# Kernel optimization log

Hardware: AMD Instinct MI355X
Metric: run time of the kernel (lower is better)

The kernel has to match this reference:

```python
import jax, jax.numpy as jnp
import numpy as np

NUM_HEADS = 16
HEAD_DIM = 64  # hidden_size 1024 / 16 heads


def setup_inputs() -> dict:
    key = jax.random.key(0)
    k1, k2 = jax.random.split(key)
    B, S, D = 2, 2048, 1024
    hidden_states = jax.random.normal(k1, (B, S, D), dtype=jnp.float32)
    # fast_qkv: bias-free fused qkv projection + separate q/v biases (init zeros in torch)
    W_qkv = jax.random.normal(k2, (D, 3 * D), dtype=jnp.float32) * (1.0 / np.sqrt(D))
    q_bias = jnp.zeros((D,), dtype=jnp.float32)
    v_bias = jnp.zeros((D,), dtype=jnp.float32)
    return {"hidden_states": hidden_states, "W_qkv": W_qkv, "q_bias": q_bias, "v_bias": v_bias}


def reference(hidden_states, W_qkv, q_bias, v_bias):
    B, S, D = hidden_states.shape
    H, hd = NUM_HEADS, HEAD_DIM
    qkv = hidden_states @ W_qkv                      # (B,S,3D)
    q, k, v = jnp.split(qkv, 3, axis=-1)
    q = q + q_bias
    v = v + v_bias
    # (B,S,H,hd)
    q = q.reshape(B, S, H, hd)
    k = k.reshape(B, S, H, hd)
    v = v.reshape(B, S, H, hd)
    q = q / jnp.sqrt(jnp.asarray(hd, dtype=q.dtype))
    # full (B,H,S,S) score tensor, softmax in fp32 then cast back (matches torch)
    scores = jnp.einsum('bqhd,bkhd->bhqk', q, k)
    probs = jax.nn.softmax(scores.astype(jnp.float32), axis=-1).astype(v.dtype)
    ctx = jnp.einsum('bhqk,bkhd->bqhd', probs, v)    # (B,S,H,hd)
    return ctx.reshape(B, S, D)
```

## Files before the change

kernel.cpp:

```cpp
#include <hip/hip_runtime.h>
#include <hip/hip_bf16.h>

typedef _Float16 half_t;
typedef _Float16 h8 __attribute__((ext_vector_type(8)));
typedef _Float16 h4 __attribute__((ext_vector_type(4)));
typedef float f32x4 __attribute__((ext_vector_type(4)));
typedef float f4 __attribute__((ext_vector_type(4)));

#define DEVI __device__ __forceinline__

constexpr int NB = 2;
constexpr int S  = 2048;
constexpr int DM = 1024;
constexpr int NH = 16;
constexpr int HD = 64;
constexpr long M = (long)NB * S;
constexpr int N3 = 3 * DM;

DEVI f32x4 mfma16(h8 a, h8 b, f32x4 c) {
  return __builtin_amdgcn_mfma_f32_16x16x32_f16(a, b, c, 0, 0, 0);
}
DEVI f32x4 mfma16h(h4 a, h4 b, f32x4 c) {
  return __builtin_amdgcn_mfma_f32_16x16x16f16(a, b, c, 0, 0, 0);
}
DEVI h8 ld8h(const half_t* p) { return *(const h8*)p; }

#if __has_builtin(__builtin_amdgcn_exp2f)
DEVI float ex2(float x) { return __builtin_amdgcn_exp2f(x); }
#else
DEVI float ex2(float x) { float r; asm("v_exp_f32 %0, %1" : "=v"(r) : "v"(x)); return r; }
#endif

DEVI void gl_lds16(const half_t* g, half_t* l) {
  __builtin_amdgcn_global_load_lds(
      (const __attribute__((address_space(1))) void*)g,
      (__attribute__((address_space(3))) void*)l, 16, 0, 0);
}

__global__ void convert_h(const float* __restrict__ in, half_t* __restrict__ out) {
  const long i = ((long)blockIdx.x * 256 + threadIdx.x) * 8;
  const f4 a = *(const f4*)(in + i), b = *(const f4*)(in + i + 4);
  h8 r;
  #pragma unroll
  for (int k = 0; k < 4; k++) { r[k] = (half_t)a[k]; r[4 + k] = (half_t)b[k]; }
  *(h8*)(out + i) = r;
}

__global__ void transpose_w(const float* __restrict__ in, half_t* __restrict__ out) {
  __shared__ float tile[32][33];
  const int c0 = blockIdx.x * 32, r0 = blockIdx.y * 32;
  const int x = threadIdx.x, y = threadIdx.y;
  #pragma unroll
  for (int i = 0; i < 32; i += 8) tile[y + i][x] = in[(long)(r0 + y + i) * N3 + c0 + x];
  __syncthreads();
  #pragma unroll
  for (int i = 0; i < 32; i += 8)
    out[(long)(c0 + y + i) * DM + r0 + x] = (half_t)tile[x][y + i];
}

__global__ void transpose_v(const half_t* __restrict__ vb, half_t* __restrict__ vt) {
  __shared__ half_t tile[32][33];
  const int b = blockIdx.z >> 4, h = blockIdx.z & 15;
  const int d0 = blockIdx.x * 32, s0 = blockIdx.y * 32;
  const int x = threadIdx.x, y = threadIdx.y;
  const half_t* ip = vb + (long)b * S * DM + h * HD;
  half_t* op = vt + (long)(b * NH + h) * HD * S;
  #pragma unroll
  for (int i = 0; i < 32; i += 8) tile[y + i][x] = ip[(long)(s0 + y + i) * DM + d0 + x];
  __syncthreads();
  #pragma unroll
  for (int i = 0; i < 32; i += 8) op[(long)(d0 + y + i) * S + s0 + x] = tile[x][y + i];
}

__global__ __launch_bounds__(256) void qkv_gemm(
    const half_t* __restrict__ A, const half_t* __restrict__ Bt,
    const float* __restrict__ qbias, const float* __restrict__ vbias,
    half_t* __restrict__ Qf, half_t* __restrict__ Kf, half_t* __restrict__ Vb)
{
  constexpr int BM = 128, BN = 128, BK = 32;
  __shared__ alignas(16) half_t As[BM * BK];
  __shared__ alignas(16) half_t Bs[BN * BK];
  const int t = threadIdx.x, lane = t & 63, wave = t >> 6;
  const int quad = lane >> 4, l16 = lane & 15;
  const int id = blockIdx.x, xcd = id & 7, jj = id >> 3;
  const int m0 = (xcd * 4 + (jj & 3)) * BM;
  const int n0 = (jj >> 2) * BN;
  const int wm = (wave & 1) * 64, wn = (wave >> 1) * 64;

  const half_t* aP0 = A  + (long)(m0 + (t >> 2)) * DM + (t & 3) * 8;
  const half_t* aP1 = aP0 + (long)64 * DM;
  const half_t* bP0 = Bt + (long)(n0 + (t >> 2)) * DM + (t & 3) * 8;
  const half_t* bP1 = bP0 + (long)64 * DM;
  half_t* asW = As + wave * 512;
  half_t* bsW = Bs + wave * 512;

  f32x4 acc[4][4] = {};

  for (int k0 = 0; k0 < DM; k0 += BK) {
    __syncthreads();
    gl_lds16(aP0 + k0, asW);
    gl_lds16(aP1 + k0, asW + 2048);
    gl_lds16(bP0 + k0, bsW);
    gl_lds16(bP1 + k0, bsW + 2048);
    __builtin_amdgcn_s_waitcnt(0);
    __syncthreads();

    h8 af[4], bfr[4];
    #pragma unroll
    for (int i = 0; i < 4; i++) af[i]  = ld8h(&As[(wm + i * 16 + l16) * BK + quad * 8]);
    #pragma unroll
    for (int j = 0; j < 4; j++) bfr[j] = ld8h(&Bs[(wn + j * 16 + l16) * BK + quad * 8]);
    #pragma unroll
    for (int i = 0; i < 4; i++)
      #pragma unroll
      for (int j = 0; j < 4; j++)
        acc[i][j] = mfma16(af[i], bfr[j], acc[i][j]);
  }

  #pragma unroll
  for (int i = 0; i < 4; i++) {
    #pragma unroll
    for (int j = 0; j < 4; j++) {
      const int n = n0 + wn + j * 16 + l16;
      #pragma unroll
      for (int r = 0; r < 4; r++) {
        const long m = m0 + wm + i * 16 + quad * 4 + r;
        const float cv = acc[i][j][r];
        if (n < DM) {
          Qf[m * DM + n] = (half_t)((cv + qbias[n]) * 0.1803368801f);
        } else if (n < 2 * DM) {
          Kf[m * DM + (n - DM)] = (half_t)cv;
        } else {
          const int nv = n - 2 * DM;
          Vb[m * DM + nv] = (half_t)(cv + vbias[nv]);
        }
      }
    }
  }
}

__global__ __launch_bounds__(256) void attn(
    const half_t* __restrict__ Qf, const half_t* __restrict__ Kf,
    const half_t* __restrict__ Vt, float* __restrict__ out)
{
  constexpr int LK = 72, LV = 72;
  __shared__ alignas(16) half_t Ks[64 * LK];
  __shared__ alignas(16) half_t Vs[64 * LV];

  const int bh = blockIdx.y, b = bh >> 4, h = bh & 15;
  const int qt = blockIdx.x;
  const int t = threadIdx.x, lane = t & 63, wave = t >> 6;
  const int quad = lane >> 4, l16 = lane & 15;

  const long qrow0 = (long)b * S + qt * 128 + wave * 32;
  const half_t* qg = Qf + qrow0 * DM + h * HD;
  const half_t* kg = Kf + (long)b * S * DM + h * HD;
  const half_t* vg = Vt + (long)bh * HD * S;

  h8 bq[2][2];
  #pragma unroll
  for (int qi = 0; qi < 2; qi++)
    #pragma unroll
    for (int dh = 0; dh < 2; dh++)
      bq[qi][dh] = ld8h(&qg[(long)(qi * 16 + l16) * DM + dh * 32 + quad * 8]);

  const int r0s = t >> 3, c0s = (t & 7) * 8;
  const int r1s = 32 + r0s;
  h8 kreg[2], vreg[2];
  kreg[0] = ld8h(&kg[(long)r0s * DM + c0s]);
  kreg[1] = ld8h(&kg[(long)r1s * DM + c0s]);
  vreg[0] = ld8h(&vg[(long)r0s * S + c0s]);
  vreg[1] = ld8h(&vg[(long)r1s * S + c0s]);

  const f32x4 z4 = {0.f, 0.f, 0.f, 0.f};
  const h4 vones = {(half_t)1.f, (half_t)1.f, (half_t)1.f, (half_t)1.f};

  f32x4 O[2][4] = {};
  f32x4 lacc[2] = {};

  for (int kt = 0; kt < S / 64; ++kt) {
    __syncthreads();
    *(h8*)&Ks[r0s * LK + c0s] = kreg[0];
    *(h8*)&Ks[r1s * LK + c0s] = kreg[1];
    *(h8*)&Vs[r0s * LV + c0s] = vreg[0];
    *(h8*)&Vs[r1s * LV + c0s] = vreg[1];
    __syncthreads();

    if (kt < S / 64 - 1) {
      const long ko = (long)(kt + 1) * 64;
      kreg[0] = ld8h(&kg[(ko + r0s) * DM + c0s]);
      kreg[1] = ld8h(&kg[(ko + r1s) * DM + c0s]);
      vreg[0] = ld8h(&vg[(long)r0s * S + ko + c0s]);
      vreg[1] = ld8h(&vg[(long)r1s * S + ko + c0s]);
    }

    h4 pa[2][4];
    #pragma unroll
    for (int g = 0; g < 4; g++) {
      const h8 kf0 = ld8h(&Ks[(g * 16 + l16) * LK + quad * 8]);
      const h8 kf1 = ld8h(&Ks[(g * 16 + l16) * LK + 32 + quad * 8]);
      #pragma unroll
      for (int qi = 0; qi < 2; qi++) {
        f32x4 sc = mfma16(kf0, bq[qi][0], z4);
        sc = mfma16(kf1, bq[qi][1], sc);
        h4 pk;
        #pragma unroll
        for (int r = 0; r < 4; r++) pk[r] = (half_t)ex2(sc[r]);
        pa[qi][g] = pk;
      }
    }

    #pragma unroll
    for (int g = 0; g < 4; g++) {
      lacc[0] = mfma16h(pa[0][g], vones, lacc[0]);
      lacc[1] = mfma16h(pa[1][g], vones, lacc[1]);
    }

    #pragma unroll
    for (int j = 0; j < 4; j++) {
      #pragma unroll
      for (int g = 0; g < 4; g++) {
        const h4 vf = *(const h4*)&Vs[(j * 16 + l16) * LV + g * 16 + quad * 4];
        O[0][j] = mfma16h(pa[0][g], vf, O[0][j]);
        O[1][j] = mfma16h(pa[1][g], vf, O[1][j]);
      }
    }
  }

  #pragma unroll
  for (int qi = 0; qi < 2; qi++) {
    #pragma unroll
    for (int r = 0; r < 4; r++) {
      const float linv = 1.f / lacc[qi][r];
      const long srow = qrow0 + qi * 16 + quad * 4 + r;
      #pragma unroll
      for (int j = 0; j < 4; j++)
        out[srow * DM + h * HD + j * 16 + l16] = O[qi][j][r] * linv;
    }
  }
}

extern "C" void kernel_launch(void* const* d_in, const int* in_sizes, int n_in,
                              void* d_out, int out_size, void* d_ws, size_t ws_size,
                              hipStream_t stream) {
  (void)in_sizes; (void)n_in; (void)out_size; (void)ws_size;
  const float* hidden = (const float*)d_in[0];
  const float* W      = (const float*)d_in[1];
  const float* qbias  = (const float*)d_in[2];
  const float* vbias  = (const float*)d_in[3];
  float* out = (float*)d_out;

  half_t* ws = (half_t*)d_ws;
  half_t* Hb = ws;
  half_t* Wt = Hb + M * DM;
  half_t* Qf = Wt + (long)N3 * DM;
  half_t* Kf = Qf + M * DM;
  half_t* Vt = Kf + M * DM;

  half_t* Vb = (half_t*)d_out;

  convert_h<<<(int)(M * DM / (256 * 8)), 256, 0, stream>>>(hidden, Hb);
  transpose_w<<<dim3(N3 / 32, DM / 32), dim3(32, 8), 0, stream>>>(W, Wt);
  qkv_gemm<<<(N3 / 128) * (int)(M / 128), 256, 0, stream>>>(Hb, Wt, qbias, vbias, Qf, Kf, Vb);
  transpose_v<<<dim3(HD / 32, S / 32, NB * NH), dim3(32, 8), 0, stream>>>(Vb, Vt);
  attn<<<dim3(S / 128, NB * NH), 256, 0, stream>>>(Qf, Kf, Vt, out);
}
```

Measured before the change: 180.2 us.

## Load K/V fragments directly from global memory, drop LDS staging and barriers

The attention kernel no longer stages K and V tiles through shared memory with a register prefetch and two block barriers per iteration. Each wave now reads its MFMA operand fragments for K and V straight from global memory, relying on L1/L2 caching since all four waves read the same tile. This removes LDS traffic and synchronisation but multiplies global/cache load requests by the wave count. It also loses the explicit one-tile-ahead prefetch, so load latency may be exposed.

```diff
diff --git a/kernel.cpp b/kernel.cpp
--- a/kernel.cpp
+++ b/kernel.cpp
@@ -143,10 +143,6 @@
     const half_t* __restrict__ Qf, const half_t* __restrict__ Kf,
     const half_t* __restrict__ Vt, float* __restrict__ out)
 {
-  constexpr int LK = 72, LV = 72;
-  __shared__ alignas(16) half_t Ks[64 * LK];
-  __shared__ alignas(16) half_t Vs[64 * LV];
-
   const int bh = blockIdx.y, b = bh >> 4, h = bh & 15;
   const int qt = blockIdx.x;
   const int t = threadIdx.x, lane = t & 63, wave = t >> 6;
@@ -154,8 +150,8 @@
 
   const long qrow0 = (long)b * S + qt * 128 + wave * 32;
   const half_t* qg = Qf + qrow0 * DM + h * HD;
-  const half_t* kg = Kf + (long)b * S * DM + h * HD;
-  const half_t* vg = Vt + (long)bh * HD * S;
+  const half_t* kfb = Kf + ((long)b * S + l16) * DM + h * HD + quad * 8;
+  const half_t* vfb = Vt + (long)bh * HD * S + (long)l16 * S + quad * 4;
 
   h8 bq[2][2];
   #pragma unroll
@@ -164,14 +160,6 @@
     for (int dh = 0; dh < 2; dh++)
       bq[qi][dh] = ld8h(&qg[(long)(qi * 16 + l16) * DM + dh * 32 + quad * 8]);
 
-  const int r0s = t >> 3, c0s = (t & 7) * 8;
-  const int r1s = 32 + r0s;
-  h8 kreg[2], vreg[2];
-  kreg[0] = ld8h(&kg[(long)r0s * DM + c0s]);
-  kreg[1] = ld8h(&kg[(long)r1s * DM + c0s]);
-  vreg[0] = ld8h(&vg[(long)r0s * S + c0s]);
-  vreg[1] = ld8h(&vg[(long)r1s * S + c0s]);
-
   const f32x4 z4 = {0.f, 0.f, 0.f, 0.f};
   const h4 vones = {(half_t)1.f, (half_t)1.f, (half_t)1.f, (half_t)1.f};
 
@@ -179,30 +167,28 @@
   f32x4 lacc[2] = {};
 
   for (int kt = 0; kt < S / 64; ++kt) {
-    __syncthreads();
-    *(h8*)&Ks[r0s * LK + c0s] = kreg[0];
-    *(h8*)&Ks[r1s * LK + c0s] = kreg[1];
-    *(h8*)&Vs[r0s * LV + c0s] = vreg[0];
-    *(h8*)&Vs[r1s * LV + c0s] = vreg[1];
-    __syncthreads();
-
-    if (kt < S / 64 - 1) {
-      const long ko = (long)(kt + 1) * 64;
-      kreg[0] = ld8h(&kg[(ko + r0s) * DM + c0s]);
-      kreg[1] = ld8h(&kg[(ko + r1s) * DM + c0s]);
-      vreg[0] = ld8h(&vg[(long)r0s * S + ko + c0s]);
-      vreg[1] = ld8h(&vg[(long)r1s * S + ko + c0s]);
-    }
+    const long k0 = (long)kt * 64;
+
+    h8 kf[4][2];
+    #pragma unroll
+    for (int g = 0; g < 4; g++) {
+      kf[g][0] = ld8h(kfb + (k0 + g * 16) * DM);
+      kf[g][1] = ld8h(kfb + (k0 + g * 16) * DM + 32);
+    }
+    h4 vf[4][4];
+    #pragma unroll
+    for (int j = 0; j < 4; j++)
+      #pragma unroll
+      for (int g = 0; g < 4; g++)
+        vf[j][g] = *(const h4*)(vfb + (long)(j * 16) * S + k0 + g * 16);
 
     h4 pa[2][4];
     #pragma unroll
     for (int g = 0; g < 4; g++) {
-      const h8 kf0 = ld8h(&Ks[(g * 16 + l16) * LK + quad * 8]);
-      const h8 kf1 = ld8h(&Ks[(g * 16 + l16) * LK + 32 + quad * 8]);
       #pragma unroll
       for (int qi = 0; qi < 2; qi++) {
-        f32x4 sc = mfma16(kf0, bq[qi][0], z4);
-        sc = mfma16(kf1, bq[qi][1], sc);
+        f32x4 sc = mfma16(kf[g][0], bq[qi][0], z4);
+        sc = mfma16(kf[g][1], bq[qi][1], sc);
         h4 pk;
         #pragma unroll
         for (int r = 0; r < 4; r++) pk[r] = (half_t)ex2(sc[r]);
@@ -220,9 +206,8 @@
     for (int j = 0; j < 4; j++) {
       #pragma unroll
       for (int g = 0; g < 4; g++) {
-        const h4 vf = *(const h4*)&Vs[(j * 16 + l16) * LV + g * 16 + quad * 4];
-        O[0][j] = mfma16h(pa[0][g], vf, O[0][j]);
-        O[1][j] = mfma16h(pa[1][g], vf, O[1][j]);
+        O[0][j] = mfma16h(pa[0][g], vf[j][g], O[0][j]);
+        O[1][j] = mfma16h(pa[1][g], vf[j][g], O[1][j]);
       }
     }
   }
```

Result: slower. 297.5 us (+65.1%).

## Halve attention query tile per block, merge prep kernels, pack exp conversions

Applied to the files above, without the earlier changes.

The attention kernel now gives each wave 16 query rows instead of 32, so each block covers 64 queries and twice as many blocks are launched. This should improve occupancy and CU fill, at the cost of loading every K/V tile twice as often per query. The hidden-state conversion and weight transpose are merged into one launch to save a kernel launch. Probabilities are converted to fp16 with packed round-toward-zero conversions.

```diff
diff --git a/kernel.cpp b/kernel.cpp
--- a/kernel.cpp
+++ b/kernel.cpp
@@ -4,6 +4,7 @@
 typedef _Float16 half_t;
 typedef _Float16 h8 __attribute__((ext_vector_type(8)));
 typedef _Float16 h4 __attribute__((ext_vector_type(4)));
+typedef _Float16 h2 __attribute__((ext_vector_type(2)));
 typedef float f32x4 __attribute__((ext_vector_type(4)));
 typedef float f4 __attribute__((ext_vector_type(4)));
 
@@ -31,31 +32,39 @@
 DEVI float ex2(float x) { float r; asm("v_exp_f32 %0, %1" : "=v"(r) : "v"(x)); return r; }
 #endif
 
+DEVI h2 pk2(float a, float b) {
+  auto r = __builtin_amdgcn_cvt_pkrtz(a, b);
+  h2 o; __builtin_memcpy(&o, &r, sizeof(o)); return o;
+}
+
 DEVI void gl_lds16(const half_t* g, half_t* l) {
   __builtin_amdgcn_global_load_lds(
       (const __attribute__((address_space(1))) void*)g,
       (__attribute__((address_space(3))) void*)l, 16, 0, 0);
 }
 
-__global__ void convert_h(const float* __restrict__ in, half_t* __restrict__ out) {
-  const long i = ((long)blockIdx.x * 256 + threadIdx.x) * 8;
-  const f4 a = *(const f4*)(in + i), b = *(const f4*)(in + i + 4);
-  h8 r;
-  #pragma unroll
-  for (int k = 0; k < 4; k++) { r[k] = (half_t)a[k]; r[4 + k] = (half_t)b[k]; }
-  *(h8*)(out + i) = r;
-}
-
-__global__ void transpose_w(const float* __restrict__ in, half_t* __restrict__ out) {
+__global__ void prep(const float* __restrict__ hidden, half_t* __restrict__ Hb,
+                     const float* __restrict__ W, half_t* __restrict__ Wt) {
   __shared__ float tile[32][33];
-  const int c0 = blockIdx.x * 32, r0 = blockIdx.y * 32;
-  const int x = threadIdx.x, y = threadIdx.y;
-  #pragma unroll
-  for (int i = 0; i < 32; i += 8) tile[y + i][x] = in[(long)(r0 + y + i) * N3 + c0 + x];
-  __syncthreads();
-  #pragma unroll
-  for (int i = 0; i < 32; i += 8)
-    out[(long)(c0 + y + i) * DM + r0 + x] = (half_t)tile[x][y + i];
+  const int id = blockIdx.x, t = threadIdx.x;
+  if (id < 2048) {
+    const long i = ((long)id * 256 + t) * 8;
+    const f4 a = *(const f4*)(hidden + i), b = *(const f4*)(hidden + i + 4);
+    h8 r;
+    #pragma unroll
+    for (int k = 0; k < 4; k++) { r[k] = (half_t)a[k]; r[4 + k] = (half_t)b[k]; }
+    *(h8*)(Hb + i) = r;
+  } else {
+    const int id2 = id - 2048;
+    const int c0 = (id2 % 96) * 32, r0 = (id2 / 96) * 32;
+    const int x = t & 31, y = t >> 5;
+    #pragma unroll
+    for (int i = 0; i < 32; i += 8) tile[y + i][x] = W[(long)(r0 + y + i) * N3 + c0 + x];
+    __syncthreads();
+    #pragma unroll
+    for (int i = 0; i < 32; i += 8)
+      Wt[(long)(c0 + y + i) * DM + r0 + x] = (half_t)tile[x][y + i];
+  }
 }
 
 __global__ void transpose_v(const half_t* __restrict__ vb, half_t* __restrict__ vt) {
@@ -152,17 +161,15 @@
   const int t = threadIdx.x, lane = t & 63, wave = t >> 6;
   const int quad = lane >> 4, l16 = lane & 15;
 
-  const long qrow0 = (long)b * S + qt * 128 + wave * 32;
+  const long qrow0 = (long)b * S + qt * 64 + wave * 16;
   const half_t* qg = Qf + qrow0 * DM + h * HD;
   const half_t* kg = Kf + (long)b * S * DM + h * HD;
   const half_t* vg = Vt + (long)bh * HD * S;
 
-  h8 bq[2][2];
-  #pragma unroll
-  for (int qi = 0; qi < 2; qi++)
-    #pragma unroll
-    for (int dh = 0; dh < 2; dh++)
-      bq[qi][dh] = ld8h(&qg[(long)(qi * 16 + l16) * DM + dh * 32 + quad * 8]);
+  h8 bq[2];
+  #pragma unroll
+  for (int dh = 0; dh < 2; dh++)
+    bq[dh] = ld8h(&qg[(long)l16 * DM + dh * 32 + quad * 8]);
 
   const int r0s = t >> 3, c0s = (t & 7) * 8;
   const int r1s = 32 + r0s;
@@ -175,8 +182,8 @@
   const f32x4 z4 = {0.f, 0.f, 0.f, 0.f};
   const h4 vones = {(half_t)1.f, (half_t)1.f, (half_t)1.f, (half_t)1.f};
 
-  f32x4 O[2][4] = {};
-  f32x4 lacc[2] = {};
+  f32x4 O[4] = {};
+  f32x4 lacc = {};
 
   for (int kt = 0; kt < S / 64; ++kt) {
     __syncthreads();
@@ -194,49 +201,39 @@
       vreg[1] = ld8h(&vg[(long)r1s * S + ko + c0s]);
     }
 
-    h4 pa[2][4];
+    h4 pa[4];
     #pragma unroll
     for (int g = 0; g < 4; g++) {
       const h8 kf0 = ld8h(&Ks[(g * 16 + l16) * LK + quad * 8]);
       const h8 kf1 = ld8h(&Ks[(g * 16 + l16) * LK + 32 + quad * 8]);
-      #pragma unroll
-      for (int qi = 0; qi < 2; qi++) {
-        f32x4 sc = mfma16(kf0, bq[qi][0], z4);
-        sc = mfma16(kf1, bq[qi][1], sc);
-        h4 pk;
-        #pragma unroll
-        for (int r = 0; r < 4; r++) pk[r] = (half_t)ex2(sc[r]);
-        pa[qi][g] = pk;
-      }
-    }
-
-    #pragma unroll
-    for (int g = 0; g < 4; g++) {
-      lacc[0] = mfma16h(pa[0][g], vones, lacc[0]);
-      lacc[1] = mfma16h(pa[1][g], vones, lacc[1]);
-    }
+      f32x4 sc = mfma16(kf0, bq[0], z4);
+      sc = mfma16(kf1, bq[1], sc);
+      const h2 lo = pk2(ex2(sc[0]), ex2(sc[1]));
+      const h2 hi = pk2(ex2(sc[2]), ex2(sc[3]));
+      union { h4 v; h2 p[2]; } u; u.p[0] = lo; u.p[1] = hi;
+      pa[g] = u.v;
+    }
+
+    #pragma unroll
+    for (int g = 0; g < 4; g++) lacc = mfma16h(pa[g], vones, lacc);
 
     #pragma unroll
     for (int j = 0; j < 4; j++) {
       #pragma unroll
       for (int g = 0; g < 4; g++) {
         const h4 vf = *(const h4*)&Vs[(j * 16 + l16) * LV + g * 16 + quad * 4];
-        O[0][j] = mfma16h(pa[0][g], vf, O[0][j]);
-        O[1][j] = mfma16h(pa[1][g], vf, O[1][j]);
+        O[j] = mfma16h(pa[g], vf, O[j]);
       }
     }
   }
 
   #pragma unroll
-  for (int qi = 0; qi < 2; qi++) {
-    #pragma unroll
-    for (int r = 0; r < 4; r++) {
-      const float linv = 1.f / lacc[qi][r];
-      const long srow = qrow0 + qi * 16 + quad * 4 + r;
-      #pragma unroll
-      for (int j = 0; j < 4; j++)
-        out[srow * DM + h * HD + j * 16 + l16] = O[qi][j][r] * linv;
-    }
+  for (int r = 0; r < 4; r++) {
+    const float linv = 1.f / lacc[r];
+    const long srow = qrow0 + quad * 4 + r;
+    #pragma unroll
+    for (int j = 0; j < 4; j++)
+      out[srow * DM + h * HD + j * 16 + l16] = O[j][r] * linv;
   }
 }
 
@@ -259,9 +256,8 @@
 
   half_t* Vb = (half_t*)d_out;
 
-  convert_h<<<(int)(M * DM / (256 * 8)), 256, 0, stream>>>(hidden, Hb);
-  transpose_w<<<dim3(N3 / 32, DM / 32), dim3(32, 8), 0, stream>>>(W, Wt);
+  prep<<<2048 + 3072, 256, 0, stream>>>(hidden, Hb, W, Wt);
   qkv_gemm<<<(N3 / 128) * (int)(M / 128), 256, 0, stream>>>(Hb, Wt, qbias, vbias, Qf, Kf, Vb);
   transpose_v<<<dim3(HD / 32, S / 32, NB * NH), dim3(32, 8), 0, stream>>>(Vb, Vt);
-  attn<<<dim3(S / 128, NB * NH), 256, 0, stream>>>(Qf, Kf, Vt, out);
-}
+  attn<<<dim3(S / 64, NB * NH), 256, 0, stream>>>(Qf, Kf, Vt, out);
+}
```

Result: slower. 186.4 us (+3.4%).
